# Optimization experiments

Measured on AMD Instinct MI355X. Metric: run time of the kernel, lower is better.

## Reference

```python
import jax, jax.numpy as jnp
import numpy as np

B, T, C = 8, 1024, 768
H, DH = 12, 64  # n_heads, head_size


def setup_inputs() -> dict:
    key = jax.random.key(0)
    ks = jax.random.split(key, 6)
    s_in = 1.0 / np.sqrt(C)
    s_pr = 1.0 / np.sqrt(H * DH)
    x = jax.random.normal(ks[0], (B, T, C), dtype=jnp.float32)
    Wq = jax.random.uniform(ks[1], (H, C, DH), minval=-s_in, maxval=s_in, dtype=jnp.float32)
    Wk = jax.random.uniform(ks[2], (H, C, DH), minval=-s_in, maxval=s_in, dtype=jnp.float32)
    Wv = jax.random.uniform(ks[3], (H, C, DH), minval=-s_in, maxval=s_in, dtype=jnp.float32)
    Wp = jax.random.uniform(ks[4], (H * DH, C), minval=-s_pr, maxval=s_pr, dtype=jnp.float32)
    bp = jax.random.uniform(ks[5], (C,), minval=-s_pr, maxval=s_pr, dtype=jnp.float32)
    return {"x": x, "Wq": Wq, "Wk": Wk, "Wv": Wv, "Wp": Wp, "bp": bp}


def reference(x, Wq, Wk, Wv, Wp, bp):
    Bx, Tx, Cx = x.shape
    # per-head projections (all heads batched): [B,T,C] x [H,C,D] -> [B,H,T,D]
    q = jnp.einsum('btc,hcd->bhtd', x, Wq)
    k = jnp.einsum('btc,hcd->bhtd', x, Wk)
    v = jnp.einsum('btc,hcd->bhtd', x, Wv)
    scale = DH ** -0.5
    scores = jnp.einsum('bhtd,bhsd->bhts', q, k) * scale  # [B,H,T,T]
    causal = jnp.tril(jnp.ones((Tx, Tx), dtype=bool))
    scores = jnp.where(causal, scores, -jnp.inf)
    weights = jax.nn.softmax(scores, axis=-1)
    # dropout is identity in eval mode (p=0)
    out = jnp.einsum('bhts,bhsd->bhtd', weights, v)  # [B,H,T,D]
    out = out.transpose(0, 2, 1, 3).reshape(Bx, Tx, H * DH)  # concat heads
    return out @ Wp + bp
```

## Files before the change

kernel.cpp:

```cpp
#include <hip/hip_runtime.h>
#include <hip/hip_bf16.h>
#include <cstdint>

#define B_  8
#define T_  1024
#define C_  768
#define H_  12
#define DH_ 64

#define BM 128
#define BN 128
#define BK 64

typedef __attribute__((ext_vector_type(8))) short short8v;
typedef __attribute__((ext_vector_type(4))) short short4v;
typedef __attribute__((ext_vector_type(4))) float f32x4;

static __device__ __forceinline__ short f2bf(float x) {
    __hip_bfloat16 h = __float2bfloat16(x);
    return *reinterpret_cast<const short*>(&h);
}

static __device__ __forceinline__ void gload16(const short* g, short* l) {
    __builtin_amdgcn_global_load_lds(
        (const __attribute__((address_space(1))) unsigned int*)g,
        (__attribute__((address_space(3))) unsigned int*)l, 16, 0, 0);
}

__global__ __launch_bounds__(256) void x_to_bf16(
        const float* __restrict__ x, short* __restrict__ xb)
{
    const size_t i = ((size_t)blockIdx.x * 256 + threadIdx.x) * 8;
    const float4 a = *(const float4*)(x + i);
    const float4 b = *(const float4*)(x + i + 4);
    short8v o;
    o[0] = f2bf(a.x); o[1] = f2bf(a.y); o[2] = f2bf(a.z); o[3] = f2bf(a.w);
    o[4] = f2bf(b.x); o[5] = f2bf(b.y); o[6] = f2bf(b.z); o[7] = f2bf(b.w);
    *(short8v*)(xb + i) = o;
}

__global__ __launch_bounds__(256) void w_transpose(
        const float* __restrict__ Wq, const float* __restrict__ Wk,
        const float* __restrict__ Wv, short* __restrict__ wt)
{
    const int z = blockIdx.z;
    const float* W = (z == 0) ? Wq : ((z == 1) ? Wk : Wv);
    short* dst = wt + (size_t)z * C_ * C_;
    const int c0 = blockIdx.x * 64;
    const int h  = blockIdx.y;
    __shared__ float tile[64][65];
    const int tid = threadIdx.x;
    const int r = tid >> 2, seg = tid & 3;

    const float* src = W + ((size_t)h * C_ + c0 + r) * 64 + seg * 16;
    #pragma unroll
    for (int u = 0; u < 4; ++u) {
        const float4 v = *(const float4*)(src + u * 4);
        tile[r][seg * 16 + u * 4 + 0] = v.x;
        tile[r][seg * 16 + u * 4 + 1] = v.y;
        tile[r][seg * 16 + u * 4 + 2] = v.z;
        tile[r][seg * 16 + u * 4 + 3] = v.w;
    }
    __syncthreads();
    short* o = dst + ((size_t)h * 64 + r) * C_ + c0 + seg * 16;
    short8v o0, o1;
    #pragma unroll
    for (int jj = 0; jj < 8; ++jj) o0[jj] = f2bf(tile[seg * 16 + jj][r]);
    #pragma unroll
    for (int jj = 0; jj < 8; ++jj) o1[jj] = f2bf(tile[seg * 16 + 8 + jj][r]);
    *(short8v*)(o)     = o0;
    *(short8v*)(o + 8) = o1;
}

__global__ __launch_bounds__(256) void wp_transpose(
        const float* __restrict__ Wp, short* __restrict__ wpt)
{
    const int n0 = blockIdx.x * 64;
    const int c0 = blockIdx.y * 64;
    __shared__ float tile[64][65];
    const int tid = threadIdx.x;
    const int r = tid >> 2, seg = tid & 3;

    const float* src = Wp + ((size_t)(c0 + r)) * C_ + n0 + seg * 16;
    #pragma unroll
    for (int u = 0; u < 4; ++u) {
        const float4 v = *(const float4*)(src + u * 4);
        tile[r][seg * 16 + u * 4 + 0] = v.x;
        tile[r][seg * 16 + u * 4 + 1] = v.y;
        tile[r][seg * 16 + u * 4 + 2] = v.z;
        tile[r][seg * 16 + u * 4 + 3] = v.w;
    }
    __syncthreads();
    short* o = wpt + ((size_t)(n0 + r)) * C_ + c0 + seg * 16;
    short8v o0, o1;
    #pragma unroll
    for (int jj = 0; jj < 8; ++jj) o0[jj] = f2bf(tile[seg * 16 + jj][r]);
    #pragma unroll
    for (int jj = 0; jj < 8; ++jj) o1[jj] = f2bf(tile[seg * 16 + 8 + jj][r]);
    *(short8v*)(o)     = o0;
    *(short8v*)(o + 8) = o1;
}


__global__ __launch_bounds__(256) void qkv_mfma(
        const short* __restrict__ xb, const short* __restrict__ wt,
        short* __restrict__ qb, short* __restrict__ kb, short* __restrict__ vb)
{
    const int z = blockIdx.z;
    const short* Bt = wt + (size_t)z * C_ * C_;
    short* out = (z == 0) ? qb : ((z == 1) ? kb : vb);
    const float osc = (z == 0) ? 0.125f : 1.0f;

    const int n0 = blockIdx.x * BN;
    const int m0 = blockIdx.y * BM;

    __shared__ short As[BM * BK];
    __shared__ short Bs[BN * BK];

    const int tid = threadIdx.x;
    const int w = tid >> 6, l = tid & 63, lg = l >> 4, lc = l & 15;
    const int wr = w >> 1, wc = w & 1;
    const int tmod8 = (tid & 7) * 8;

    f32x4 acc[4][4];
    #pragma unroll
    for (int i = 0; i < 4; ++i)
        #pragma unroll
        for (int j = 0; j < 4; ++j) acc[i][j] = (f32x4){0.f, 0.f, 0.f, 0.f};

    for (int k0 = 0; k0 < C_; k0 += BK) {
        #pragma unroll
        for (int it = 0; it < 4; ++it) {
            const int t = it * 256 + tid;
            const int row = t >> 3;
            gload16(xb + ((size_t)(m0 + row)) * C_ + k0 + tmod8, As + t * 8);
            gload16(Bt + ((size_t)(n0 + row)) * C_ + k0 + tmod8, Bs + t * 8);
        }
        __syncthreads();
        #pragma unroll
        for (int ks = 0; ks < 2; ++ks) {
            short8v af[4], bfv[4];
            #pragma unroll
            for (int i = 0; i < 4; ++i)
                af[i] = *(const short8v*)(As + (wr * 64 + i * 16 + lc) * BK + ks * 32 + lg * 8);
            #pragma unroll
            for (int j = 0; j < 4; ++j)
                bfv[j] = *(const short8v*)(Bs + (wc * 64 + j * 16 + lc) * BK + ks * 32 + lg * 8);
            #pragma unroll
            for (int i = 0; i < 4; ++i)
                #pragma unroll
                for (int j = 0; j < 4; ++j)
                    acc[i][j] = __builtin_amdgcn_mfma_f32_16x16x32_bf16(af[i], bfv[j], acc[i][j], 0, 0, 0);
        }
        __syncthreads();
    }

    const int h = blockIdx.x * 2 + wc;
    #pragma unroll
    for (int i = 0; i < 4; ++i) {
        #pragma unroll
        for (int r = 0; r < 4; ++r) {
            const int m  = m0 + wr * 64 + i * 16 + lg * 4 + r;
            const int bb = m >> 10, tt = m & (T_ - 1);
            short* op = out + (((size_t)(bb * H_ + h)) * T_ + tt) * 64;
            #pragma unroll
            for (int j = 0; j < 4; ++j)
                op[j * 16 + lc] = f2bf(acc[i][j][r] * osc);
        }
    }
}

__global__ __launch_bounds__(256) void proj_mfma(
        const short* __restrict__ ab, const short* __restrict__ wpt,
        const float* __restrict__ bp, float* __restrict__ out)
{
    const int n0 = blockIdx.x * BN;
    const int m0 = blockIdx.y * BM;

    __shared__ short As[BM * BK];
    __shared__ short Bs[BN * BK];

    const int tid = threadIdx.x;
    const int w = tid >> 6, l = tid & 63, lg = l >> 4, lc = l & 15;
    const int wr = w >> 1, wc = w & 1;
    const int tmod8 = (tid & 7) * 8;

    f32x4 acc[4][4];
    #pragma unroll
    for (int i = 0; i < 4; ++i)
        #pragma unroll
        for (int j = 0; j < 4; ++j) acc[i][j] = (f32x4){0.f, 0.f, 0.f, 0.f};

    for (int k0 = 0; k0 < C_; k0 += BK) {
        #pragma unroll
        for (int it = 0; it < 4; ++it) {
            const int t = it * 256 + tid;
            const int row = t >> 3;
            gload16(ab  + ((size_t)(m0 + row)) * C_ + k0 + tmod8, As + t * 8);
            gload16(wpt + ((size_t)(n0 + row)) * C_ + k0 + tmod8, Bs + t * 8);
        }
        __syncthreads();
        #pragma unroll
        for (int ks = 0; ks < 2; ++ks) {
            short8v af[4], bfv[4];
            #pragma unroll
            for (int i = 0; i < 4; ++i)
                af[i] = *(const short8v*)(As + (wr * 64 + i * 16 + lc) * BK + ks * 32 + lg * 8);
            #pragma unroll
            for (int j = 0; j < 4; ++j)
                bfv[j] = *(const short8v*)(Bs + (wc * 64 + j * 16 + lc) * BK + ks * 32 + lg * 8);
            #pragma unroll
            for (int i = 0; i < 4; ++i)
                #pragma unroll
                for (int j = 0; j < 4; ++j)
                    acc[i][j] = __builtin_amdgcn_mfma_f32_16x16x32_bf16(af[i], bfv[j], acc[i][j], 0, 0, 0);
        }
        __syncthreads();
    }

    float bias[4];
    #pragma unroll
    for (int j = 0; j < 4; ++j) bias[j] = bp[n0 + wc * 64 + j * 16 + lc];
    #pragma unroll
    for (int i = 0; i < 4; ++i) {
        #pragma unroll
        for (int r = 0; r < 4; ++r) {
            const int m = m0 + wr * 64 + i * 16 + lg * 4 + r;
            float* op = out + (size_t)m * C_ + n0 + wc * 64 + lc;
            #pragma unroll
            for (int j = 0; j < 4; ++j)
                op[j * 16] = acc[i][j][r] + bias[j];
        }
    }
}

__global__ __launch_bounds__(256) void v_transpose(
        const __hip_bfloat16* __restrict__ vb, __hip_bfloat16* __restrict__ vt)
{
    const int t0 = blockIdx.x * 64;
    const int h  = blockIdx.y;
    const int b  = blockIdx.z;
    __shared__ short tile[64][72];
    const int tid = threadIdx.x;
    const int r   = tid >> 2;
    const int seg = tid & 3;

    const short* src = (const short*)vb +
        (((size_t)(b * H_ + h)) * T_ + t0 + r) * 64 + seg * 16;
    *(short8v*)(&tile[r][seg * 16])     = *(const short8v*)(src);
    *(short8v*)(&tile[r][seg * 16 + 8]) = *(const short8v*)(src + 8);
    __syncthreads();

    short* dst = (short*)vt +
        (((size_t)(b * H_ + h)) * 64 + r) * T_ + t0 + seg * 16;
    short8v o0, o1;
    #pragma unroll
    for (int j = 0; j < 8; ++j) o0[j] = tile[seg * 16 + j][r];
    #pragma unroll
    for (int j = 0; j < 8; ++j) o1[j] = tile[seg * 16 + 8 + j][r];
    *(short8v*)(dst)     = o0;
    *(short8v*)(dst + 8) = o1;
}

__global__ __launch_bounds__(256) void attn_mfma(
        const __hip_bfloat16* __restrict__ qb,
        const __hip_bfloat16* __restrict__ kb,
        const __hip_bfloat16* __restrict__ vt,
        short* __restrict__ ab)
{
    const int bx = blockIdx.x;
    const int h  = blockIdx.y;
    const int b  = blockIdx.z;
    const int tid = threadIdx.x;
    const int w  = tid >> 6;
    const int l  = tid & 63;
    const int lg = l >> 4;
    const int lc = l & 15;

    const size_t headRow = ((size_t)(b * H_ + h)) * T_;
    const size_t vtRow   = ((size_t)(b * H_ + h)) * 64;

    __shared__ short p_s[4][16][72];

    #pragma unroll
    for (int phase = 0; phase < 2; ++phase) {
        const int qt = (phase == 0) ? bx : (15 - bx);
        const int q0 = qt * 64 + w * 16;

        short8v aq0, aq1;
        {
            const short* qp = (const short*)qb + (headRow + q0 + lc) * 64 + lg * 8;
            aq0 = *(const short8v*)(qp);
            aq1 = *(const short8v*)(qp + 32);
        }

        float m_r[4], l_r[4];
        f32x4 o_acc[4];
        #pragma unroll
        for (int r = 0; r < 4; ++r) { m_r[r] = -1e30f; l_r[r] = 0.0f; }
        #pragma unroll
        for (int n = 0; n < 4; ++n) o_acc[n] = (f32x4){0.f, 0.f, 0.f, 0.f};

        for (int kt = 0; kt <= qt; ++kt) {
            const int kv0 = kt * 64;

            short8v bk0[4], bk1[4], bv0[4], bv1[4];
            #pragma unroll
            for (int n = 0; n < 4; ++n) {
                const short* kp = (const short*)kb + (headRow + kv0 + n * 16 + lc) * 64 + lg * 8;
                bk0[n] = *(const short8v*)(kp);
                bk1[n] = *(const short8v*)(kp + 32);
                const short* vp = (const short*)vt + (vtRow + n * 16 + lc) * T_ + kv0 + lg * 8;
                bv0[n] = *(const short8v*)(vp);
                bv1[n] = *(const short8v*)(vp + 32);
            }

            f32x4 s[4];
            #pragma unroll
            for (int n = 0; n < 4; ++n) {
                f32x4 a2 = (f32x4){0.f, 0.f, 0.f, 0.f};
                a2 = __builtin_amdgcn_mfma_f32_16x16x32_bf16(aq0, bk0[n], a2, 0, 0, 0);
                a2 = __builtin_amdgcn_mfma_f32_16x16x32_bf16(aq1, bk1[n], a2, 0, 0, 0);
                s[n] = a2;
            }

            if (kt == qt) {
                #pragma unroll
                for (int n = 0; n < 4; ++n) {
                    const int kvg = kv0 + n * 16 + lc;
                    #pragma unroll
                    for (int r = 0; r < 4; ++r) {
                        const int qg = q0 + lg * 4 + r;
                        if (kvg > qg) s[n][r] = -1e30f;
                    }
                }
            }

            float p[4][4];
            float pscale[4];
            #pragma unroll
            for (int r = 0; r < 4; ++r) {
                float tm = fmaxf(fmaxf(s[0][r], s[1][r]), fmaxf(s[2][r], s[3][r]));
                #pragma unroll
                for (int mk = 8; mk >= 1; mk >>= 1) tm = fmaxf(tm, __shfl_xor(tm, mk, 16));
                const float mnew = fmaxf(m_r[r], tm);
                pscale[r] = __expf(m_r[r] - mnew);
                float ps = 0.f;
                #pragma unroll
                for (int n = 0; n < 4; ++n) { p[n][r] = __expf(s[n][r] - mnew); ps += p[n][r]; }
                #pragma unroll
                for (int mk = 8; mk >= 1; mk >>= 1) ps += __shfl_xor(ps, mk, 16);
                l_r[r] = l_r[r] * pscale[r] + ps;
                m_r[r] = mnew;
            }
            #pragma unroll
            for (int n = 0; n < 4; ++n)
                #pragma unroll
                for (int r = 0; r < 4; ++r) o_acc[n][r] *= pscale[r];

            #pragma unroll
            for (int n = 0; n < 4; ++n)
                #pragma unroll
                for (int r = 0; r < 4; ++r)
                    p_s[w][lg * 4 + r][n * 16 + lc] = f2bf(p[n][r]);

            const short* prow = &p_s[w][lc][lg * 8];
            short8v pa0 = *(const short8v*)(prow);
            short8v pa1 = *(const short8v*)(prow + 32);
            #pragma unroll
            for (int n = 0; n < 4; ++n) {
                o_acc[n] = __builtin_amdgcn_mfma_f32_16x16x32_bf16(pa0, bv0[n], o_acc[n], 0, 0, 0);
                o_acc[n] = __builtin_amdgcn_mfma_f32_16x16x32_bf16(pa1, bv1[n], o_acc[n], 0, 0, 0);
            }
        }

        #pragma unroll
        for (int r = 0; r < 4; ++r) {
            const float inv = 1.0f / l_r[r];
            const int q = q0 + lg * 4 + r;
            short* op = ab + ((size_t)(b * T_) + q) * C_ + h * 64 + lc;
            #pragma unroll
            for (int n = 0; n < 4; ++n) op[n * 16] = f2bf(o_acc[n][r] * inv);
        }
    }
}


extern "C" void kernel_launch(void* const* d_in, const int* in_sizes, int n_in,
                              void* d_out, int out_size, void* d_ws, size_t ws_size,
                              hipStream_t stream)
{
    const float* x  = (const float*)d_in[0];
    const float* Wq = (const float*)d_in[1];
    const float* Wk = (const float*)d_in[2];
    const float* Wv = (const float*)d_in[3];
    const float* Wp = (const float*)d_in[4];
    const float* bp = (const float*)d_in[5];
    float* out = (float*)d_out;

    char* ws = (char*)d_ws;
    const size_t NE = (size_t)B_ * T_ * C_;
    const size_t BF = NE * sizeof(short);
    short* xb  = (short*)(ws);
    short* qb  = (short*)(ws + BF);
    short* kb  = (short*)(ws + 2 * BF);
    short* vb  = (short*)(ws + 3 * BF);
    short* vt  = (short*)(ws + 4 * BF);
    short* ab  = (short*)(ws + 5 * BF);
    short* wt  = (short*)(ws + 6 * BF);
    short* wpt = (short*)(ws + 6 * BF + 3 * C_ * C_ * 2);

    x_to_bf16<<<dim3(NE / (256 * 8)), dim3(256), 0, stream>>>(x, xb);
    w_transpose<<<dim3(12, 12, 3), dim3(256), 0, stream>>>(Wq, Wk, Wv, wt);
    wp_transpose<<<dim3(12, 12), dim3(256), 0, stream>>>(Wp, wpt);

    qkv_mfma<<<dim3(C_ / BN, (B_ * T_) / BM, 3), dim3(256), 0, stream>>>(
        xb, wt, qb, kb, vb);

    v_transpose<<<dim3(T_ / 64, H_, B_), dim3(256), 0, stream>>>(
        (const __hip_bfloat16*)vb, (__hip_bfloat16*)vt);

    attn_mfma<<<dim3(8, H_, B_), dim3(256), 0, stream>>>(
        (const __hip_bfloat16*)qb, (const __hip_bfloat16*)kb,
        (const __hip_bfloat16*)vt, ab);

    proj_mfma<<<dim3(C_ / BN, (B_ * T_) / BM), dim3(256), 0, stream>>>(
        ab, wpt, bp, out);
}
```

Baseline: 276.7 us.

## Stage K/V tiles in double-buffered LDS and remap attention blocks

The attention kernel now has all four waves share K and V tiles. These are loaded once per block into double-buffered LDS with async global-to-LDS loads, and the next tile is prefetched while the current one is computed. Previously each wave fetched the tiles from global memory itself. The launch is flattened to a 1D grid with a swizzled block index, so blocks working on the same (batch, head) are grouped for L2 locality. This adds a barrier per KV iteration and possible LDS bank conflicts on the 128-byte-stride row reads.

```diff
diff --git a/kernel.cpp b/kernel.cpp
--- a/kernel.cpp
+++ b/kernel.cpp
@@ -268,9 +268,11 @@
         const __hip_bfloat16* __restrict__ vt,
         short* __restrict__ ab)
 {
-    const int bx = blockIdx.x;
-    const int h  = blockIdx.y;
-    const int b  = blockIdx.z;
+    const int ii = blockIdx.x;
+    const int wg = (ii % 96) * 8 + (ii / 96);
+    const int bx = wg & 7;
+    const int h  = (wg >> 3) % H_;
+    const int b  = wg / (8 * H_);
     const int tid = threadIdx.x;
     const int w  = tid >> 6;
     const int l  = tid & 63;
@@ -279,7 +281,11 @@
 
     const size_t headRow = ((size_t)(b * H_ + h)) * T_;
     const size_t vtRow   = ((size_t)(b * H_ + h)) * 64;
-
+    const short* kbp = (const short*)kb;
+    const short* vtp = (const short*)vt;
+
+    __shared__ short Ks[2][64 * 64];
+    __shared__ short Vs[2][64 * 64];
     __shared__ short p_s[4][16][72];
 
     #pragma unroll
@@ -301,30 +307,43 @@
         #pragma unroll
         for (int n = 0; n < 4; ++n) o_acc[n] = (f32x4){0.f, 0.f, 0.f, 0.f};
 
+        #pragma unroll
+        for (int u = 0; u < 2; ++u) {
+            const int t = u * 256 + tid;
+            const int row = t >> 3, c8 = (t & 7) * 8;
+            gload16(kbp + (headRow + row) * 64 + c8, &Ks[0][t * 8]);
+            gload16(vtp + (vtRow + row) * T_ + c8, &Vs[0][t * 8]);
+        }
+        __syncthreads();
+
+        int cur = 0;
         for (int kt = 0; kt <= qt; ++kt) {
-            const int kv0 = kt * 64;
-
-            short8v bk0[4], bk1[4], bv0[4], bv1[4];
+            if (kt < qt) {
+                const int kv1 = (kt + 1) * 64;
+                #pragma unroll
+                for (int u = 0; u < 2; ++u) {
+                    const int t = u * 256 + tid;
+                    const int row = t >> 3, c8 = (t & 7) * 8;
+                    gload16(kbp + (headRow + kv1 + row) * 64 + c8, &Ks[cur ^ 1][t * 8]);
+                    gload16(vtp + (vtRow + row) * T_ + kv1 + c8, &Vs[cur ^ 1][t * 8]);
+                }
+            }
+            const short* Kc = Ks[cur];
+            const short* Vc = Vs[cur];
+
+            f32x4 s[4];
             #pragma unroll
             for (int n = 0; n < 4; ++n) {
-                const short* kp = (const short*)kb + (headRow + kv0 + n * 16 + lc) * 64 + lg * 8;
-                bk0[n] = *(const short8v*)(kp);
-                bk1[n] = *(const short8v*)(kp + 32);
-                const short* vp = (const short*)vt + (vtRow + n * 16 + lc) * T_ + kv0 + lg * 8;
-                bv0[n] = *(const short8v*)(vp);
-                bv1[n] = *(const short8v*)(vp + 32);
-            }
-
-            f32x4 s[4];
-            #pragma unroll
-            for (int n = 0; n < 4; ++n) {
+                const short8v bk0 = *(const short8v*)(Kc + (n * 16 + lc) * 64 + lg * 8);
+                const short8v bk1 = *(const short8v*)(Kc + (n * 16 + lc) * 64 + 32 + lg * 8);
                 f32x4 a2 = (f32x4){0.f, 0.f, 0.f, 0.f};
-                a2 = __builtin_amdgcn_mfma_f32_16x16x32_bf16(aq0, bk0[n], a2, 0, 0, 0);
-                a2 = __builtin_amdgcn_mfma_f32_16x16x32_bf16(aq1, bk1[n], a2, 0, 0, 0);
+                a2 = __builtin_amdgcn_mfma_f32_16x16x32_bf16(aq0, bk0, a2, 0, 0, 0);
+                a2 = __builtin_amdgcn_mfma_f32_16x16x32_bf16(aq1, bk1, a2, 0, 0, 0);
                 s[n] = a2;
             }
 
             if (kt == qt) {
+                const int kv0 = kt * 64;
                 #pragma unroll
                 for (int n = 0; n < 4; ++n) {
                     const int kvg = kv0 + n * 16 + lc;
@@ -365,13 +384,19 @@
                     p_s[w][lg * 4 + r][n * 16 + lc] = f2bf(p[n][r]);
 
             const short* prow = &p_s[w][lc][lg * 8];
-            short8v pa0 = *(const short8v*)(prow);
-            short8v pa1 = *(const short8v*)(prow + 32);
+            const short8v pa0 = *(const short8v*)(prow);
+            const short8v pa1 = *(const short8v*)(prow + 32);
+
             #pragma unroll
             for (int n = 0; n < 4; ++n) {
-                o_acc[n] = __builtin_amdgcn_mfma_f32_16x16x32_bf16(pa0, bv0[n], o_acc[n], 0, 0, 0);
-                o_acc[n] = __builtin_amdgcn_mfma_f32_16x16x32_bf16(pa1, bv1[n], o_acc[n], 0, 0, 0);
+                const short8v bv0 = *(const short8v*)(Vc + (n * 16 + lc) * 64 + lg * 8);
+                const short8v bv1 = *(const short8v*)(Vc + (n * 16 + lc) * 64 + 32 + lg * 8);
+                o_acc[n] = __builtin_amdgcn_mfma_f32_16x16x32_bf16(pa0, bv0, o_acc[n], 0, 0, 0);
+                o_acc[n] = __builtin_amdgcn_mfma_f32_16x16x32_bf16(pa1, bv1, o_acc[n], 0, 0, 0);
             }
+
+            __syncthreads();
+            cur ^= 1;
         }
 
         #pragma unroll
@@ -420,7 +445,7 @@
     v_transpose<<<dim3(T_ / 64, H_, B_), dim3(256), 0, stream>>>(
         (const __hip_bfloat16*)vb, (__hip_bfloat16*)vt);
 
-    attn_mfma<<<dim3(8, H_, B_), dim3(256), 0, stream>>>(
+    attn_mfma<<<dim3(8 * H_ * B_), dim3(256), 0, stream>>>(
         (const __hip_bfloat16*)qb, (const __hip_bfloat16*)kb,
         (const __hip_bfloat16*)vt, ab);
 
```

Result: faster. 241.7 us (-12.6%).
